# Performance work log

Measured on AMD Instinct MI355X. Metric: run time of the kernel, lower is better.

The kernel has to match this reference:

```python
import jax, jax.numpy as jnp
import numpy as np

FILTER_SIZE = 1024
NUM_HEADS = 16
D_HEAD = FILTER_SIZE // NUM_HEADS
LN_EPS = 1e-5


def setup_inputs() -> dict:
    key = jax.random.key(0)
    ks = jax.random.split(key, 10)
    B, T, D = 2, 2048, FILTER_SIZE
    s = 1.0 / np.sqrt(D)
    return {
        "x": jax.random.normal(ks[0], (B, T, D), dtype=jnp.float32),
        "Wq": jax.random.normal(ks[1], (D, D), dtype=jnp.float32) * s,
        "bq": jnp.zeros((D,), dtype=jnp.float32),
        "Wk": jax.random.normal(ks[2], (D, D), dtype=jnp.float32) * s,
        "bk": jnp.zeros((D,), dtype=jnp.float32),
        "Wv": jax.random.normal(ks[3], (D, D), dtype=jnp.float32) * s,
        "bv": jnp.zeros((D,), dtype=jnp.float32),
        "Wo": jax.random.normal(ks[4], (D, D), dtype=jnp.float32) * s,
        "bo": jnp.zeros((D,), dtype=jnp.float32),
        "gamma": jnp.ones((D,), dtype=jnp.float32),
        "beta": jnp.zeros((D,), dtype=jnp.float32),
    }


def reference(x, Wq, bq, Wk, bk, Wv, bv, Wo, bo, gamma, beta):
    B, T, D = x.shape
    H, Dh = NUM_HEADS, D_HEAD
    # Note: source splits features as (d_head, heads) with heads LAST.
    q = (x @ Wq.T + bq).reshape(B, T, Dh, H)
    k = (x @ Wk.T + bk).reshape(B, T, Dh, H)
    v = (x @ Wv.T + bv).reshape(B, T, Dh, H)
    scale = 1.0 / np.sqrt(Dh).astype(np.float32)
    # scores: (B, H, T, T)
    scores = jnp.einsum("bidh,bjdh->bhij", q, k) * scale
    attn = jax.nn.softmax(scores, axis=-1)  # dropout is identity in eval
    out = jnp.einsum("bhij,bjdh->bidh", attn, v)  # (B, T, Dh, H)
    out = out.reshape(B, T, D)  # matches permute(0,2,3,1).reshape in torch
    out = out @ Wo.T + bo
    out = out + x
    mu = jnp.mean(out, axis=-1, keepdims=True)
    var = jnp.var(out, axis=-1, keepdims=True)
    out = (out - mu) * jax.lax.rsqrt(var + LN_EPS) * gamma + beta
    return out
```

## Files before the change

### kernel.cpp

```cpp
#include <hip/hip_runtime.h>
#include <stdint.h>

#define T_SEQ 2048
#define D_MODEL 1024
#define NH 16
#define DH 64
#define NROWS 4096

typedef __bf16 bf16x8 __attribute__((ext_vector_type(8)));
typedef float floatx4 __attribute__((ext_vector_type(4)));
typedef short short4v __attribute__((ext_vector_type(4)));
typedef short short8v __attribute__((ext_vector_type(8)));

#define AS1 __attribute__((address_space(1)))
#define AS3 __attribute__((address_space(3)))

static __device__ __forceinline__ void gl2lds16(const unsigned short* g, unsigned short* s) {
    __builtin_amdgcn_global_load_lds((const AS1 unsigned int*)g, (AS3 unsigned int*)s, 16, 0, 0);
}

static __device__ __forceinline__ unsigned short f32_bf16(float f) {
    union { float f; unsigned int u; } c; c.f = f;
    unsigned int u = c.u;
    u = u + 0x7FFFu + ((u >> 16) & 1u);
    return (unsigned short)(u >> 16);
}

static __device__ __forceinline__ unsigned int pack2_bf16(float a, float b) {
    return (unsigned int)f32_bf16(a) | ((unsigned int)f32_bf16(b) << 16);
}

static __device__ __forceinline__ floatx4 mfma16(bf16x8 a, bf16x8 b, floatx4 c) {
    return __builtin_amdgcn_mfma_f32_16x16x32_bf16(a, b, c, 0, 0, 0);
}

static __device__ __forceinline__ floatx4 mfma16k16(short4v a, short4v b, floatx4 c) {
#if defined(__HIP_DEVICE_COMPILE__)
    return __builtin_amdgcn_mfma_f32_16x16x16bf16_1k(a, b, c, 0, 0, 0);
#else
    (void)a; (void)b;
    return c;
#endif
}

#define QSCALE 0.1803368801111204f
#define EXP2_SHIFT 10.0f
#define WAITCNT_VM(n) (0x0F70 | (n))

__global__ __launch_bounds__(256) void k_conv_all(const float* __restrict__ x,
                                                  const float* __restrict__ Wq,
                                                  const float* __restrict__ Wk,
                                                  const float* __restrict__ Wv,
                                                  const float* __restrict__ Wo,
                                                  unsigned short* __restrict__ x_bf,
                                                  unsigned short* __restrict__ wqkv_bf,
                                                  unsigned short* __restrict__ wo_bf) {
    int b = blockIdx.x, t = threadIdx.x;
    if (b < 4096) {
        int i = b * 1024 + t * 4;
        float4 v = *(const float4*)(x + i);
        uint2 o;
        o.x = pack2_bf16(v.x, v.y);
        o.y = pack2_bf16(v.z, v.w);
        *(uint2*)(x_bf + i) = o;
    } else if (b < 7168) {
        int idx = b - 4096;
        int tensor = idx >> 10, np = idx & 1023;
        const float* src = tensor == 0 ? Wq : tensor == 1 ? Wk : Wv;
        int f = (np & 63) * 16 + (np >> 6);
        int c = t * 4;
        float4 v = *(const float4*)(src + (long)f * D_MODEL + c);
        uint2 o;
        o.x = pack2_bf16(v.x, v.y);
        o.y = pack2_bf16(v.z, v.w);
        *(uint2*)(wqkv_bf + ((long)tensor * D_MODEL + np) * D_MODEL + c) = o;
    } else {
        int n = b - 7168;
        int fp = t * 4;
        const float* row = Wo + (long)n * D_MODEL;
        unsigned short o[4];
        #pragma unroll
        for (int k = 0; k < 4; k++) {
            int f = fp + k;
            o[k] = f32_bf16(row[(f & 63) * 16 + (f >> 6)]);
        }
        *(uint2*)(wo_bf + (long)n * D_MODEL + fp) = *(const uint2*)o;
    }
}

template <int BN, int MODE>
__global__ __launch_bounds__(256) void k_gemm(const unsigned short* __restrict__ A,
                                              const unsigned short* __restrict__ W,
                                              const float* __restrict__ b0,
                                              const float* __restrict__ b1,
                                              const float* __restrict__ b2,
                                              const float* __restrict__ resid,
                                              unsigned short* __restrict__ out_bf,
                                              unsigned short* __restrict__ vtg,
                                              float* __restrict__ out_f32) {
    constexpr int NT = BN / 32;
    constexpr int NCB = BN / 32;
    constexpr int NDMA = 4 + NCB;
    __shared__ unsigned short lds_a[2 * 128 * 64];
    __shared__ unsigned short lds_b[2 * BN * 64];
    const int tid = threadIdx.x;
    const int w = tid >> 6, l = tid & 63;
    const int lrow = l & 15, lq = l >> 4;
    const int wm = (w >> 1) * 64, wn = (w & 1) * (BN / 2);
    const int L = blockIdx.x;
    const int bx = (L & 7) * 4 + ((L >> 3) & 3);
    const int by = L >> 5;
    const long am0 = (long)bx * 128;
    const long wn0 = (long)by * BN;

    floatx4 acc[4][NT] = {};
    const int grow = l >> 3;
    const int gcol = ((l & 7) ^ grow) * 8;
    const int sw8 = (lrow & 7);

    auto stage = [&](int ki, int sel) {
        unsigned short* la = lds_a + sel * 8192;
        unsigned short* lb = lds_b + sel * (BN * 64);
        int k0 = ki * 64;
        #pragma unroll
        for (int c = 0; c < 4; c++) {
            int chunk = w * 4 + c;
            gl2lds16(A + (am0 + chunk * 8 + grow) * D_MODEL + k0 + gcol, la + chunk * 512);
        }
        #pragma unroll
        for (int c = 0; c < NCB; c++) {
            int chunk = w * NCB + c;
            gl2lds16(W + (wn0 + chunk * 8 + grow) * D_MODEL + k0 + gcol, lb + chunk * 512);
        }
    };

    stage(0, 0);

    for (int i = 0; i < 16; i++) {
        const int cur = i & 1;
        if (i < 15) {
            stage(i + 1, 1 - cur);
            __builtin_amdgcn_s_waitcnt(WAITCNT_VM(NDMA));
        } else {
            __builtin_amdgcn_s_waitcnt(WAITCNT_VM(0));
        }
        __builtin_amdgcn_s_barrier();

        const unsigned short* la = lds_a + cur * 8192;
        const unsigned short* lb = lds_b + cur * (BN * 64);
        bf16x8 af[4][2], bf[NT][2];
        #pragma unroll
        for (int mt = 0; mt < 4; mt++)
            #pragma unroll
            for (int ks = 0; ks < 2; ks++)
                af[mt][ks] = *(const bf16x8*)(la + (wm + mt * 16 + lrow) * 64 +
                                              (((ks * 4 + lq) ^ sw8) * 8));
        #pragma unroll
        for (int nt = 0; nt < NT; nt++)
            #pragma unroll
            for (int ks = 0; ks < 2; ks++)
                bf[nt][ks] = *(const bf16x8*)(lb + (wn + nt * 16 + lrow) * 64 +
                                              (((ks * 4 + lq) ^ sw8) * 8));
        #pragma unroll
        for (int mt = 0; mt < 4; mt++)
            #pragma unroll
            for (int nt = 0; nt < NT; nt++)
                #pragma unroll
                for (int ks = 0; ks < 2; ks++)
                    acc[mt][nt] = mfma16(af[mt][ks], bf[nt][ks], acc[mt][nt]);
        __builtin_amdgcn_s_barrier();
    }

    if (MODE == 0) {
        int tensor = by >> 3;
        int nbase = (by & 7) * 128;
        const float* bias = tensor == 0 ? b0 : tensor == 1 ? b1 : b2;
        float scale = tensor == 0 ? QSCALE : 1.0f;
        if (tensor < 2) {
            unsigned short* outt = out_bf + (size_t)tensor * (32u * T_SEQ * DH);
            #pragma unroll
            for (int mt = 0; mt < 4; mt++) {
                #pragma unroll
                for (int nt = 0; nt < NT; nt++) {
                    int n = nbase + wn + nt * 16 + lrow;
                    int h = n >> 6, d = n & 63;
                    float bb = bias[d * 16 + h];
                    #pragma unroll
                    for (int r = 0; r < 4; r++) {
                        int row = (int)am0 + wm + mt * 16 + lq * 4 + r;
                        float v = (acc[mt][nt][r] + bb) * scale;
                        int b = row >> 11, i = row & 2047;
                        long idx = ((long)(b * 16 + h) * T_SEQ + i) * DH + d;
                        outt[idx] = f32_bf16(v);
                    }
                }
            }
        } else {
            int row0 = (int)am0 + wm;
            int b = row0 >> 11;
            int blk = (row0 & 2047) >> 6;
            #pragma unroll
            for (int nt = 0; nt < NT; nt++) {
                int n = nbase + wn + nt * 16 + lrow;
                int h = n >> 6, d = n & 63;
                float bb = bias[d * 16 + h];
                long base = (((long)(b * 16 + h) * 64 + d) * 32 + blk) * 64;
                #pragma unroll
                for (int mt = 0; mt < 4; mt++) {
                    uint2 o;
                    o.x = pack2_bf16(acc[mt][nt][0] + bb, acc[mt][nt][1] + bb);
                    o.y = pack2_bf16(acc[mt][nt][2] + bb, acc[mt][nt][3] + bb);
                    *(uint2*)(vtg + base + lq * 16 + mt * 4) = o;
                }
            }
        }
    } else {
        #pragma unroll
        for (int mt = 0; mt < 4; mt++) {
            #pragma unroll
            for (int nt = 0; nt < NT; nt++) {
                int n = (int)wn0 + wn + nt * 16 + lrow;
                float bb = b0[n];
                #pragma unroll
                for (int r = 0; r < 4; r++) {
                    int row = (int)am0 + wm + mt * 16 + lq * 4 + r;
                    long idx = (long)row * D_MODEL + n;
                    out_f32[idx] = acc[mt][nt][r] + bb + resid[idx];
                }
            }
        }
    }
}

__global__ __launch_bounds__(256) void k_attn(const unsigned short* __restrict__ q_ws,
                                              const unsigned short* __restrict__ k_ws,
                                              const unsigned short* __restrict__ vtg,
                                              unsigned short* __restrict__ att) {
    __shared__ unsigned short kbuf[2 * 64 * 64];
    __shared__ unsigned short vbuf[2 * 64 * 64];
    const int tid = threadIdx.x;
    const int w = tid >> 6, l = tid & 63;
    const int lrow = l & 15, lq = l >> 4;
    const int sw = lrow & 7;
    const int L = blockIdx.x;
    const int bh = (L & 7) * 4 + ((L >> 3) & 3);
    const int i0 = (L >> 5) * 128;
    const unsigned short* kh = k_ws + (long)bh * T_SEQ * DH;
    const unsigned short* vh = vtg + (long)bh * 64 * T_SEQ;

    const int rl = l >> 3;
    const int gl = ((l & 7) ^ rl) * 8;

    bf16x8 qf[2][2];
    #pragma unroll
    for (int qt = 0; qt < 2; qt++) {
        const unsigned short* qp =
            q_ws + ((long)bh * T_SEQ + i0 + w * 32 + qt * 16 + lrow) * DH + lq * 8;
        qf[qt][0] = *(const bf16x8*)qp;
        qf[qt][1] = *(const bf16x8*)(qp + 32);
    }
    floatx4 o_acc[2][4] = {};
    floatx4 l_acc[2] = {};
    const short4v ones = {0x3F80, 0x3F80, 0x3F80, 0x3F80};

    auto stage_k = [&](int jt, int sel) {
        unsigned short* kd = kbuf + sel * 4096 + (w * 2) * 512;
        #pragma unroll
        for (int c = 0; c < 2; c++) {
            int row = w * 16 + c * 8 + rl;
            gl2lds16(kh + ((long)(jt * 64 + row)) * 64 + gl, kd + c * 512);
        }
    };
    auto stage_v = [&](int jt, int sel) {
        unsigned short* vd = vbuf + sel * 4096 + (w * 2) * 512;
        #pragma unroll
        for (int c = 0; c < 2; c++) {
            int row = w * 16 + c * 8 + rl;
            gl2lds16(vh + ((long)row * 32 + jt) * 64 + gl, vd + c * 512);
        }
    };

    auto qk = [&](const unsigned short* kb_, floatx4 (&s0)[4], floatx4 (&s1)[4]) {
        #pragma unroll
        for (int nt = 0; nt < 4; nt++) {
            const unsigned short* kp = kb_ + (nt * 16 + lrow) * 64;
            bf16x8 ka = *(const bf16x8*)(kp + ((lq ^ sw) * 8));
            bf16x8 kb = *(const bf16x8*)(kp + (((lq + 4) ^ sw) * 8));
            floatx4 c0 = {-EXP2_SHIFT, -EXP2_SHIFT, -EXP2_SHIFT, -EXP2_SHIFT};
            floatx4 c1 = c0;
            c0 = mfma16(ka, qf[0][0], c0);
            c0 = mfma16(kb, qf[0][1], c0);
            c1 = mfma16(ka, qf[1][0], c1);
            c1 = mfma16(kb, qf[1][1], c1);
            s0[nt] = c0;
            s1[nt] = c1;
        }
    };

    auto softpack = [&](floatx4 s, short4v& pf, int qt) {
        float p0 = __builtin_amdgcn_exp2f(s[0]);
        float p1 = __builtin_amdgcn_exp2f(s[1]);
        float p2 = __builtin_amdgcn_exp2f(s[2]);
        float p3 = __builtin_amdgcn_exp2f(s[3]);
        uint2 pk;
        pk.x = __builtin_amdgcn_perm(__float_as_uint(p1), __float_as_uint(p0), 0x07060302);
        pk.y = __builtin_amdgcn_perm(__float_as_uint(p3), __float_as_uint(p2), 0x07060302);
        union { uint2 u; short4v s4; } cv; cv.u = pk;
        pf = cv.s4;
        l_acc[qt] = mfma16k16(ones, pf, l_acc[qt]);
    };

    auto pv_dt = [&](const unsigned short* vb_, int dt,
                     short4v (&p0)[4], short4v (&p1)[4]) {
        const unsigned short* vp = vb_ + (dt * 16 + lrow) * 64;
        short8v v01 = *(const short8v*)(vp + (((2 * lq) ^ sw) * 8));
        short8v v23 = *(const short8v*)(vp + (((2 * lq + 1) ^ sw) * 8));
        short4v va = __builtin_shufflevector(v01, v01, 0, 1, 2, 3);
        short4v vb = __builtin_shufflevector(v01, v01, 4, 5, 6, 7);
        short4v vc = __builtin_shufflevector(v23, v23, 0, 1, 2, 3);
        short4v vd = __builtin_shufflevector(v23, v23, 4, 5, 6, 7);
        o_acc[0][dt] = mfma16k16(va, p0[0], o_acc[0][dt]);
        o_acc[0][dt] = mfma16k16(vb, p0[1], o_acc[0][dt]);
        o_acc[0][dt] = mfma16k16(vc, p0[2], o_acc[0][dt]);
        o_acc[0][dt] = mfma16k16(vd, p0[3], o_acc[0][dt]);
        o_acc[1][dt] = mfma16k16(va, p1[0], o_acc[1][dt]);
        o_acc[1][dt] = mfma16k16(vb, p1[1], o_acc[1][dt]);
        o_acc[1][dt] = mfma16k16(vc, p1[2], o_acc[1][dt]);
        o_acc[1][dt] = mfma16k16(vd, p1[3], o_acc[1][dt]);
    };

    auto tile_body = [&](const unsigned short* kb_, const unsigned short* vb_,
                         short4v (&pp0)[4], short4v (&pp1)[4],
                         short4v (&pc0)[4], short4v (&pc1)[4]) {
        floatx4 s0[4], s1[4];
        qk(kb_, s0, s1);
        #pragma unroll
        for (int dt = 0; dt < 4; dt++) {
            pv_dt(vb_, dt, pp0, pp1);
            softpack(s0[dt], pc0[dt], 0);
            softpack(s1[dt], pc1[dt], 1);
        }
    };

    short4v pA0[4], pA1[4], pB0[4], pB1[4];

    stage_k(0, 0);
    stage_k(1, 1);
    stage_v(0, 0);
    __builtin_amdgcn_s_waitcnt(WAITCNT_VM(4));
    __builtin_amdgcn_s_barrier();
    {
        floatx4 s0[4], s1[4];
        qk(kbuf, s0, s1);
        #pragma unroll
        for (int dt = 0; dt < 4; dt++) {
            softpack(s0[dt], pA0[dt], 0);
            softpack(s1[dt], pA1[dt], 1);
        }
    }
    __builtin_amdgcn_s_barrier();

    for (int t = 1; t < 31; t += 2) {
        stage_k(t + 1, (t + 1) & 1);
        stage_v(t, t & 1);
        __builtin_amdgcn_s_waitcnt(WAITCNT_VM(4));
        __builtin_amdgcn_s_barrier();
        tile_body(kbuf + (t & 1) * 4096, vbuf + ((t - 1) & 1) * 4096,
                  pA0, pA1, pB0, pB1);
        __builtin_amdgcn_s_barrier();
        stage_k(t + 2, t & 1);
        stage_v(t + 1, (t + 1) & 1);
        __builtin_amdgcn_s_waitcnt(WAITCNT_VM(4));
        __builtin_amdgcn_s_barrier();
        tile_body(kbuf + ((t + 1) & 1) * 4096, vbuf + (t & 1) * 4096,
                  pB0, pB1, pA0, pA1);
        __builtin_amdgcn_s_barrier();
    }

    stage_v(31, 1);
    __builtin_amdgcn_s_waitcnt(WAITCNT_VM(2));
    __builtin_amdgcn_s_barrier();
    tile_body(kbuf + 4096, vbuf + 0, pA0, pA1, pB0, pB1);
    __builtin_amdgcn_s_barrier();

    __builtin_amdgcn_s_waitcnt(WAITCNT_VM(0));
    __builtin_amdgcn_s_barrier();
    #pragma unroll
    for (int dt = 0; dt < 4; dt++) pv_dt(vbuf + 4096, dt, pB0, pB1);

    int h = bh & 15, b = bh >> 4;
    #pragma unroll
    for (int qt = 0; qt < 2; qt++) {
        float rl2 = 1.0f / l_acc[qt][0];
        int i = i0 + w * 32 + qt * 16 + lrow;
        unsigned short* orow = att + ((long)(b * T_SEQ + i)) * D_MODEL + h * 64;
        #pragma unroll
        for (int dt = 0; dt < 4; dt++) {
            uint2 o;
            o.x = pack2_bf16(o_acc[qt][dt][0] * rl2, o_acc[qt][dt][1] * rl2);
            o.y = pack2_bf16(o_acc[qt][dt][2] * rl2, o_acc[qt][dt][3] * rl2);
            *(uint2*)(orow + dt * 16 + lq * 4) = o;
        }
    }
}

__global__ __launch_bounds__(256) void k_ln(float* __restrict__ io,
                                            const float* __restrict__ gamma,
                                            const float* __restrict__ beta) {
    int row = blockIdx.x, t = threadIdx.x;
    float* p = io + (long)row * D_MODEL + t * 4;
    float4 v = *(float4*)p;
    float s = v.x + v.y + v.z + v.w;
    float ss = v.x * v.x + v.y * v.y + v.z * v.z + v.w * v.w;
    #pragma unroll
    for (int m = 1; m < 64; m <<= 1) {
        s += __shfl_xor(s, m);
        ss += __shfl_xor(ss, m);
    }
    __shared__ float red[8];
    if ((t & 63) == 0) { red[t >> 6] = s; red[4 + (t >> 6)] = ss; }
    __syncthreads();
    s = red[0] + red[1] + red[2] + red[3];
    ss = red[4] + red[5] + red[6] + red[7];
    float mu = s * (1.0f / 1024.0f);
    float var = ss * (1.0f / 1024.0f) - mu * mu;
    float rstd = rsqrtf(var + 1e-5f);
    float4 g = *(const float4*)(gamma + t * 4);
    float4 be = *(const float4*)(beta + t * 4);
    float4 o;
    o.x = (v.x - mu) * rstd * g.x + be.x;
    o.y = (v.y - mu) * rstd * g.y + be.y;
    o.z = (v.z - mu) * rstd * g.z + be.z;
    o.w = (v.w - mu) * rstd * g.w + be.w;
    *(float4*)p = o;
}

extern "C" void kernel_launch(void* const* d_in, const int* in_sizes, int n_in,
                              void* d_out, int out_size, void* d_ws, size_t ws_size,
                              hipStream_t stream) {
    const float* x = (const float*)d_in[0];
    const float* Wq = (const float*)d_in[1];
    const float* bq = (const float*)d_in[2];
    const float* Wk = (const float*)d_in[3];
    const float* bk = (const float*)d_in[4];
    const float* Wv = (const float*)d_in[5];
    const float* bv = (const float*)d_in[6];
    const float* Wo = (const float*)d_in[7];
    const float* bo = (const float*)d_in[8];
    const float* gamma = (const float*)d_in[9];
    const float* beta = (const float*)d_in[10];
    float* out = (float*)d_out;

    char* ws = (char*)d_ws;
    unsigned short* x_bf = (unsigned short*)(ws);
    unsigned short* wqkv_bf = (unsigned short*)(ws + ((size_t)8 << 20));
    unsigned short* wo_bf = (unsigned short*)(ws + ((size_t)14 << 20));
    unsigned short* qkv_ws = (unsigned short*)(ws + ((size_t)16 << 20));
    unsigned short* att = x_bf;

    unsigned short* q_ws = qkv_ws;
    unsigned short* k_ws = qkv_ws + (size_t)32 * T_SEQ * DH;
    unsigned short* vtg = qkv_ws + (size_t)64 * T_SEQ * DH;

    k_conv_all<<<8192, 256, 0, stream>>>(x, Wq, Wk, Wv, Wo, x_bf, wqkv_bf, wo_bf);

    k_gemm<128, 0><<<768, 256, 0, stream>>>(
        x_bf, wqkv_bf, bq, bk, bv, nullptr, qkv_ws, vtg, nullptr);

    k_attn<<<512, 256, 0, stream>>>(q_ws, k_ws, vtg, att);

    k_gemm<64, 1><<<512, 256, 0, stream>>>(
        att, wo_bf, bo, nullptr, nullptr, x, nullptr, nullptr, out);

    k_ln<<<NROWS, 256, 0, stream>>>(out, gamma, beta);
}
```

Measured before the change: 213.6 us.

## Use 16x16x32 bf16 MFMA for PV and row-sum instead of K16 variant

Replaces the 16x16x16 bf16 MFMAs in the PV product and the softmax row-sum with 16x16x32 MFMAs, halving the MFMA instruction count per tile. The V-transpose layout written by the projection epilogue is permuted so each lane's 8 consecutive keys line up with the packed probability pairs. Probabilities are packed into 8-wide vectors. This relies on the key ordering in V matching the concatenation of two score tiles, and changes register pressure and instruction scheduling.

```diff
diff --git a/kernel.cpp b/kernel.cpp
--- a/kernel.cpp
+++ b/kernel.cpp
@@ -34,13 +34,8 @@
     return __builtin_amdgcn_mfma_f32_16x16x32_bf16(a, b, c, 0, 0, 0);
 }
 
-static __device__ __forceinline__ floatx4 mfma16k16(short4v a, short4v b, floatx4 c) {
-#if defined(__HIP_DEVICE_COMPILE__)
-    return __builtin_amdgcn_mfma_f32_16x16x16bf16_1k(a, b, c, 0, 0, 0);
-#else
-    (void)a; (void)b;
-    return c;
-#endif
+static __device__ __forceinline__ bf16x8 as_bf(short8v s) {
+    union { short8v s; bf16x8 b; } u; u.s = s; return u.b;
 }
 
 #define QSCALE 0.1803368801111204f
@@ -210,7 +205,7 @@
                     uint2 o;
                     o.x = pack2_bf16(acc[mt][nt][0] + bb, acc[mt][nt][1] + bb);
                     o.y = pack2_bf16(acc[mt][nt][2] + bb, acc[mt][nt][3] + bb);
-                    *(uint2*)(vtg + base + lq * 16 + mt * 4) = o;
+                    *(uint2*)(vtg + base + (mt >> 1) * 32 + lq * 8 + (mt & 1) * 4) = o;
                 }
             }
         }
@@ -261,7 +256,8 @@
     }
     floatx4 o_acc[2][4] = {};
     floatx4 l_acc[2] = {};
-    const short4v ones = {0x3F80, 0x3F80, 0x3F80, 0x3F80};
+    const short8v ones8s = {0x3F80, 0x3F80, 0x3F80, 0x3F80, 0x3F80, 0x3F80, 0x3F80, 0x3F80};
+    const bf16x8 ones8 = as_bf(ones8s);
 
     auto stage_k = [&](int jt, int sel) {
         unsigned short* kd = kbuf + sel * 4096 + (w * 2) * 512;
@@ -297,7 +293,7 @@
         }
     };
 
-    auto softpack = [&](floatx4 s, short4v& pf, int qt) {
+    auto sp4 = [&](floatx4 s) -> short4v {
         float p0 = __builtin_amdgcn_exp2f(s[0]);
         float p1 = __builtin_amdgcn_exp2f(s[1]);
         float p2 = __builtin_amdgcn_exp2f(s[2]);
@@ -306,43 +302,41 @@
         pk.x = __builtin_amdgcn_perm(__float_as_uint(p1), __float_as_uint(p0), 0x07060302);
         pk.y = __builtin_amdgcn_perm(__float_as_uint(p3), __float_as_uint(p2), 0x07060302);
         union { uint2 u; short4v s4; } cv; cv.u = pk;
-        pf = cv.s4;
-        l_acc[qt] = mfma16k16(ones, pf, l_acc[qt]);
+        return cv.s4;
     };
 
     auto pv_dt = [&](const unsigned short* vb_, int dt,
-                     short4v (&p0)[4], short4v (&p1)[4]) {
+                     short8v (&p0)[2], short8v (&p1)[2]) {
         const unsigned short* vp = vb_ + (dt * 16 + lrow) * 64;
-        short8v v01 = *(const short8v*)(vp + (((2 * lq) ^ sw) * 8));
-        short8v v23 = *(const short8v*)(vp + (((2 * lq + 1) ^ sw) * 8));
-        short4v va = __builtin_shufflevector(v01, v01, 0, 1, 2, 3);
-        short4v vb = __builtin_shufflevector(v01, v01, 4, 5, 6, 7);
-        short4v vc = __builtin_shufflevector(v23, v23, 0, 1, 2, 3);
-        short4v vd = __builtin_shufflevector(v23, v23, 4, 5, 6, 7);
-        o_acc[0][dt] = mfma16k16(va, p0[0], o_acc[0][dt]);
-        o_acc[0][dt] = mfma16k16(vb, p0[1], o_acc[0][dt]);
-        o_acc[0][dt] = mfma16k16(vc, p0[2], o_acc[0][dt]);
-        o_acc[0][dt] = mfma16k16(vd, p0[3], o_acc[0][dt]);
-        o_acc[1][dt] = mfma16k16(va, p1[0], o_acc[1][dt]);
-        o_acc[1][dt] = mfma16k16(vb, p1[1], o_acc[1][dt]);
-        o_acc[1][dt] = mfma16k16(vc, p1[2], o_acc[1][dt]);
-        o_acc[1][dt] = mfma16k16(vd, p1[3], o_acc[1][dt]);
+        bf16x8 vg0 = *(const bf16x8*)(vp + ((lq ^ sw) * 8));
+        bf16x8 vg1 = *(const bf16x8*)(vp + (((4 + lq) ^ sw) * 8));
+        o_acc[0][dt] = mfma16(vg0, as_bf(p0[0]), o_acc[0][dt]);
+        o_acc[0][dt] = mfma16(vg1, as_bf(p0[1]), o_acc[0][dt]);
+        o_acc[1][dt] = mfma16(vg0, as_bf(p1[0]), o_acc[1][dt]);
+        o_acc[1][dt] = mfma16(vg1, as_bf(p1[1]), o_acc[1][dt]);
     };
 
     auto tile_body = [&](const unsigned short* kb_, const unsigned short* vb_,
-                         short4v (&pp0)[4], short4v (&pp1)[4],
-                         short4v (&pc0)[4], short4v (&pc1)[4]) {
+                         short8v (&pp0)[2], short8v (&pp1)[2],
+                         short8v (&pc0)[2], short8v (&pc1)[2]) {
         floatx4 s0[4], s1[4];
         qk(kb_, s0, s1);
         #pragma unroll
-        for (int dt = 0; dt < 4; dt++) {
-            pv_dt(vb_, dt, pp0, pp1);
-            softpack(s0[dt], pc0[dt], 0);
-            softpack(s1[dt], pc1[dt], 1);
-        }
-    };
-
-    short4v pA0[4], pA1[4], pB0[4], pB1[4];
+        for (int g = 0; g < 2; g++) {
+            pv_dt(vb_, 2 * g, pp0, pp1);
+            short4v t00 = sp4(s0[2 * g]);
+            short4v t10 = sp4(s1[2 * g]);
+            pv_dt(vb_, 2 * g + 1, pp0, pp1);
+            short4v t01 = sp4(s0[2 * g + 1]);
+            short4v t11 = sp4(s1[2 * g + 1]);
+            pc0[g] = __builtin_shufflevector(t00, t01, 0, 1, 2, 3, 4, 5, 6, 7);
+            pc1[g] = __builtin_shufflevector(t10, t11, 0, 1, 2, 3, 4, 5, 6, 7);
+            l_acc[0] = mfma16(ones8, as_bf(pc0[g]), l_acc[0]);
+            l_acc[1] = mfma16(ones8, as_bf(pc1[g]), l_acc[1]);
+        }
+    };
+
+    short8v pA0[2], pA1[2], pB0[2], pB1[2];
 
     stage_k(0, 0);
     stage_k(1, 1);
@@ -353,9 +347,15 @@
         floatx4 s0[4], s1[4];
         qk(kbuf, s0, s1);
         #pragma unroll
-        for (int dt = 0; dt < 4; dt++) {
-            softpack(s0[dt], pA0[dt], 0);
-            softpack(s1[dt], pA1[dt], 1);
+        for (int g = 0; g < 2; g++) {
+            short4v t00 = sp4(s0[2 * g]);
+            short4v t01 = sp4(s0[2 * g + 1]);
+            short4v t10 = sp4(s1[2 * g]);
+            short4v t11 = sp4(s1[2 * g + 1]);
+            pA0[g] = __builtin_shufflevector(t00, t01, 0, 1, 2, 3, 4, 5, 6, 7);
+            pA1[g] = __builtin_shufflevector(t10, t11, 0, 1, 2, 3, 4, 5, 6, 7);
+            l_acc[0] = mfma16(ones8, as_bf(pA0[g]), l_acc[0]);
+            l_acc[1] = mfma16(ones8, as_bf(pA1[g]), l_acc[1]);
         }
     }
     __builtin_amdgcn_s_barrier();
```

Result: faster. 202.7 us (-5.1%).
